# Kernel optimization log

Hardware: AMD Instinct MI355X
Metric: run time of the kernel (lower is better)

Reference implementation:

```python
import jax, jax.numpy as jnp
import numpy as np

N = 100000
E = 1600000
F_IN = 32
HID = 16
C_OUT = 10
K = 4


def setup_inputs() -> dict:
    key = jax.random.key(0)
    k1, k2, k3, k4, k5, k6, k7 = jax.random.split(key, 7)
    x = jax.random.normal(k1, (N, F_IN), dtype=jnp.float32)
    edge_index = jax.random.randint(k2, (2, E), 0, N, dtype=jnp.int64)
    # ChebConv weights: one [in, out] matrix per Chebyshev order k
    W1 = jax.random.normal(k3, (K, F_IN, HID), dtype=jnp.float32) / np.sqrt(F_IN)
    b1 = jax.random.normal(k4, (HID,), dtype=jnp.float32) * 0.01
    W2 = jax.random.normal(k5, (K, HID, C_OUT), dtype=jnp.float32) / np.sqrt(HID)
    b2 = jax.random.normal(k6, (C_OUT,), dtype=jnp.float32) * 0.01
    return {"x": x, "edge_index": edge_index, "W1": W1, "b1": b1, "W2": W2, "b2": b2}


def _cheb_conv(h, src, dst, norm, W, b, num_nodes):
    # Tx_0 = h; Tx_1 = L_hat h; Tx_k = 2 L_hat Tx_{k-1} - Tx_{k-2}
    def prop(v):  # v: [N, F] -> L_hat v via sparse gather/scatter
        return jax.ops.segment_sum(norm[:, None] * v[src], dst, num_segments=num_nodes)

    Tx0 = h
    out = Tx0 @ W[0]
    Tx1 = prop(h)
    out = out + Tx1 @ W[1]
    for k in range(2, W.shape[0]):
        Tx2 = 2.0 * prop(Tx1) - Tx0
        out = out + Tx2 @ W[k]
        Tx0, Tx1 = Tx1, Tx2
    return out + b


def reference(x, edge_index, W1, b1, W2, b2):
    src, dst = edge_index[0], edge_index[1]
    num_nodes = x.shape[0]
    # symmetric normalization with lambda_max = 2: L_hat = -D^{-1/2} A D^{-1/2}
    deg = jax.ops.segment_sum(jnp.ones((src.shape[0],), dtype=x.dtype), dst, num_segments=num_nodes)
    dis = jnp.where(deg > 0, jax.lax.rsqrt(jnp.maximum(deg, 1.0)), 0.0)
    norm = -dis[src] * dis[dst]
    h = _cheb_conv(x, src, dst, norm, W1, b1, num_nodes)
    h = jax.nn.relu(h)
    # dropout is identity in eval mode
    h = _cheb_conv(h, src, dst, norm, W2, b2, num_nodes)
    return jax.nn.log_softmax(h, axis=1)
```

## Files before the change

### kernel.cpp

```cpp
#include <hip/hip_runtime.h>
#include <hip/hip_bf16.h>
#include <math.h>


#define BLK 256
#define BLKP 512
#define NBUCK_MAX 256
#define CHUNK 8192
#define CAPB 16384
#define PLACE_CAP 10240

__device__ inline unsigned short f32_to_bf16_rne(float f) {
    unsigned int u = __float_as_uint(f);
    unsigned int rounding = 0x7FFFu + ((u >> 16) & 1u);
    return (unsigned short)((u + rounding) >> 16);
}
__device__ inline unsigned int pack_bf16x2(float a, float b) {
    return (unsigned int)f32_to_bf16_rne(a) | ((unsigned int)f32_to_bf16_rne(b) << 16);
}
__device__ inline void unpack8(const uint4 u, float* f) {
    const unsigned int* p = &u.x;
#pragma unroll
    for (int j = 0; j < 4; j++) {
        unsigned int w = p[j];
        f[2 * j]     = __uint_as_float(w << 16);
        f[2 * j + 1] = __uint_as_float(w & 0xFFFF0000u);
    }
}
__device__ inline void add8(const uint4 u, float* acc) {
    const unsigned int* p = &u.x;
#pragma unroll
    for (int j = 0; j < 4; j++) {
        unsigned int w = p[j];
        acc[2 * j]     += __uint_as_float(w << 16);
        acc[2 * j + 1] += __uint_as_float(w & 0xFFFF0000u);
    }
}
__device__ inline uint4 pack8(const float* r) {
    uint4 o;
    o.x = pack_bf16x2(r[0], r[1]);
    o.y = pack_bf16x2(r[2], r[3]);
    o.z = pack_bf16x2(r[4], r[5]);
    o.w = pack_bf16x2(r[6], r[7]);
    return o;
}

__device__ inline void fma8_w8(const uint4 u, float s, const float* __restrict__ W,
                               float* acc) {
    const unsigned int* p = &u.x;
#pragma unroll
    for (int q = 0; q < 4; q++) {
        float fa = __uint_as_float(p[q] << 16) * s;
        float fb = __uint_as_float(p[q] & 0xFFFF0000u) * s;
        const float* Wa = W + (2 * q) * 16;
        const float* Wb = W + (2 * q + 1) * 16;
#pragma unroll
        for (int j = 0; j < 8; j++) acc[j] += fa * Wa[j] + fb * Wb[j];
    }
}

__global__ __launch_bounds__(BLK)
void binned_scatter_kernel(const int* __restrict__ src, const int* __restrict__ dst,
                           int* __restrict__ bfill, int* __restrict__ tmp,
                           int E, int nbuck) {
    __shared__ int cnt[NBUCK_MAX];
    __shared__ int lofs[NBUCK_MAX + 1];
    __shared__ int pos[NBUCK_MAX];
    __shared__ int gbase[NBUCK_MAX];
    __shared__ int stage[CHUNK];
    __shared__ unsigned char bkt[CHUNK];

    int tid = threadIdx.x;
    int e0 = blockIdx.x * CHUNK;
    int nE = min(CHUNK, E - e0);

    for (int b = tid; b < nbuck; b += BLK) { cnt[b] = 0; pos[b] = 0; }
    __syncthreads();

    for (int i = tid; i < nE; i += BLK) {
        int d = dst[e0 + i];
        atomicAdd(&cnt[d >> 9], 1);
    }
    __syncthreads();

    {
        int v = (tid < nbuck) ? cnt[tid] : 0;
        lofs[tid] = v;
        __syncthreads();
        for (int off = 1; off < BLK; off <<= 1) {
            int t = (tid >= off) ? lofs[tid - off] : 0;
            __syncthreads();
            lofs[tid] += t;
            __syncthreads();
        }
        int incl = lofs[tid];
        __syncthreads();
        lofs[tid] = incl - v;
        if (tid == 0) lofs[nbuck] = nE;
        if (tid < nbuck && v > 0)
            gbase[tid] = tid * CAPB + atomicAdd(&bfill[tid], v);
    }
    __syncthreads();

    for (int i = tid; i < nE; i += BLK) {
        int s = src[e0 + i];
        int d = dst[e0 + i];
        int b = d >> 9;
        int slot = lofs[b] + atomicAdd(&pos[b], 1);
        stage[slot] = (s << 9) | (d & 511);
        bkt[slot] = (unsigned char)b;
    }
    __syncthreads();

    for (int i = tid; i < nE; i += BLK) {
        int b = bkt[i];
        tmp[gbase[b] + (i - lofs[b])] = stage[i];
    }
}

__global__ __launch_bounds__(BLKP)
void bucket_place_kernel(const int* __restrict__ bfill, const int* __restrict__ tmp,
                         int* __restrict__ psrc, int* __restrict__ rowbeg,
                         int* __restrict__ rowend, float* __restrict__ dis,
                         float* __restrict__ d2, float* __restrict__ inv,
                         const float* __restrict__ x, uint4* __restrict__ u0, int N) {
    __shared__ int cnt4[512 * 4];
    __shared__ int ofs[512];
    __shared__ int fill4[512 * 4];
    __shared__ int stage[PLACE_CAP];

    int b = blockIdx.x;
    int tid = threadIdx.x;
    int n0 = b << 9;
    int nn = min(512, N - n0);
    int S = b * CAPB;
    int tot = bfill[b];

    int t1 = N >> 2, t2 = N >> 1, t3 = t2 + t1;

    for (int i = tid; i < 512 * 4; i += BLKP) { cnt4[i] = 0; fill4[i] = 0; }
    __syncthreads();

    for (int i = tid; i < tot; i += BLKP) {
        int rec = tmp[S + i];
        int nl = rec & 511;
        int s = rec >> 9;
        int q = (s >= t2) ? ((s >= t3) ? 3 : 2) : ((s >= t1) ? 1 : 0);
        atomicAdd(&cnt4[nl * 4 + q], 1);
    }
    __syncthreads();

    int c0 = cnt4[tid * 4 + 0], c1 = cnt4[tid * 4 + 1];
    int c2 = cnt4[tid * 4 + 2], c3 = cnt4[tid * 4 + 3];
    int v = c0 + c1 + c2 + c3;
    cnt4[tid * 4 + 0] = 0;
    cnt4[tid * 4 + 1] = c0;
    cnt4[tid * 4 + 2] = c0 + c1;
    cnt4[tid * 4 + 3] = c0 + c1 + c2;
    ofs[tid] = v;
    __syncthreads();
    for (int off = 1; off < 512; off <<= 1) {
        int t = (tid >= off) ? ofs[tid - off] : 0;
        __syncthreads();
        ofs[tid] += t;
        __syncthreads();
    }
    int excl = ofs[tid] - v;
    __syncthreads();
    ofs[tid] = excl;
    float dn = (v > 0) ? rsqrtf((float)v) : 0.0f;
    if (tid < nn) {
        int n = n0 + tid;
        rowbeg[n] = S + excl;
        rowend[n] = S + excl + v;
        float fv = (float)v;
        dis[n] = dn;
        d2[n]  = (v > 0) ? 1.0f / fv : 0.0f;
        inv[n] = (v > 0) ? sqrtf(fv) : 0.0f;
        const float4* xr = reinterpret_cast<const float4*>(x + (size_t)n * 32);
#pragma unroll
        for (int c = 0; c < 4; c++) {
            float4 a = xr[c * 2], bb = xr[c * 2 + 1];
            float r[8] = {dn * a.x, dn * a.y, dn * a.z, dn * a.w,
                          dn * bb.x, dn * bb.y, dn * bb.z, dn * bb.w};
            u0[(size_t)n * 4 + c] = pack8(r);
        }
    }
    __syncthreads();

    if (tot <= PLACE_CAP) {
        for (int i = tid; i < tot; i += BLKP) {
            int rec = tmp[S + i];
            int nl = rec & 511;
            int s = rec >> 9;
            int q = (s >= t2) ? ((s >= t3) ? 3 : 2) : ((s >= t1) ? 1 : 0);
            int slot = ofs[nl] + cnt4[nl * 4 + q] + atomicAdd(&fill4[nl * 4 + q], 1);
            stage[slot] = s;
        }
        __syncthreads();
        for (int i = tid; i < tot; i += BLKP) psrc[S + i] = stage[i];
    } else {
        for (int i = tid; i < tot; i += BLKP) {
            int rec = tmp[S + i];
            int nl = rec & 511;
            int s = rec >> 9;
            int q = (s >= t2) ? ((s >= t3) ? 3 : 2) : ((s >= t1) ? 1 : 0);
            int slot = S + ofs[nl] + cnt4[nl * 4 + q] + atomicAdd(&fill4[nl * 4 + q], 1);
            psrc[slot] = s;
        }
    }
}

template <int C, bool HAVE_PREV>
__global__ __launch_bounds__(BLK)
void prop_u_kernel(const int* __restrict__ rowbeg, const int* __restrict__ rowend,
                   const int* __restrict__ psrc, const float* __restrict__ d2,
                   const uint4* __restrict__ vb, const uint4* __restrict__ prevb,
                   uint4* __restrict__ outb, float scale, int N) {
    int t = blockIdx.x * blockDim.x + threadIdx.x;
    int n = t / C;
    int c = t % C;
    if (n >= N) return;
    int beg = rowbeg[n];
    int end = rowend[n];
    float acc[8];
#pragma unroll
    for (int j = 0; j < 8; j++) acc[j] = 0.f;
    int i = beg;
    for (; i + 7 < end; i += 8) {
        int s0 = psrc[i],     s1 = psrc[i + 1], s2 = psrc[i + 2], s3 = psrc[i + 3];
        int s4 = psrc[i + 4], s5 = psrc[i + 5], s6 = psrc[i + 6], s7 = psrc[i + 7];
        uint4 a0 = vb[(size_t)s0 * C + c];
        uint4 a1 = vb[(size_t)s1 * C + c];
        uint4 a2 = vb[(size_t)s2 * C + c];
        uint4 a3 = vb[(size_t)s3 * C + c];
        uint4 a4 = vb[(size_t)s4 * C + c];
        uint4 a5 = vb[(size_t)s5 * C + c];
        uint4 a6 = vb[(size_t)s6 * C + c];
        uint4 a7 = vb[(size_t)s7 * C + c];
        add8(a0, acc); add8(a1, acc); add8(a2, acc); add8(a3, acc);
        add8(a4, acc); add8(a5, acc); add8(a6, acc); add8(a7, acc);
    }
    for (; i + 3 < end; i += 4) {
        int s0 = psrc[i], s1 = psrc[i + 1], s2 = psrc[i + 2], s3 = psrc[i + 3];
        uint4 a0 = vb[(size_t)s0 * C + c];
        uint4 a1 = vb[(size_t)s1 * C + c];
        uint4 a2 = vb[(size_t)s2 * C + c];
        uint4 a3 = vb[(size_t)s3 * C + c];
        add8(a0, acc); add8(a1, acc); add8(a2, acc); add8(a3, acc);
    }
    for (; i < end; i++) {
        uint4 a0 = vb[(size_t)psrc[i] * C + c];
        add8(a0, acc);
    }
    float f = -scale * d2[n];
    float r[8];
    if (HAVE_PREV) {
        float p[8];
        unpack8(prevb[(size_t)n * C + c], p);
#pragma unroll
        for (int j = 0; j < 8; j++) r[j] = f * acc[j] - p[j];
    } else {
#pragma unroll
        for (int j = 0; j < 8; j++) r[j] = f * acc[j];
    }
    outb[(size_t)n * C + c] = pack8(r);
}

__global__ __launch_bounds__(BLK)
void combine1_kernel(const float* __restrict__ x, const uint4* __restrict__ u1,
                     const uint4* __restrict__ u2, const uint4* __restrict__ u3,
                     const float* __restrict__ inv, const float* __restrict__ dis,
                     const float* __restrict__ W1, const float* __restrict__ b1,
                     uint4* __restrict__ hb, uint4* __restrict__ uh, int N) {
    __shared__ float sW[4 * 32 * 16];
    __shared__ float sb[16];
    for (int i = threadIdx.x; i < 4 * 32 * 16; i += blockDim.x) sW[i] = W1[i];
    if (threadIdx.x < 16) sb[threadIdx.x] = b1[threadIdx.x];
    __syncthreads();
    int t = blockIdx.x * blockDim.x + threadIdx.x;
    int n = t >> 1;
    int h = t & 1;
    if (n >= N) return;
    const float* sWh = sW + h * 8;
    float acc[8];
#pragma unroll
    for (int j = 0; j < 8; j++) acc[j] = sb[h * 8 + j];
    {
        const float4* in4 = reinterpret_cast<const float4*>(x + (size_t)n * 32);
#pragma unroll
        for (int q = 0; q < 8; q++) {
            float4 a = in4[q];
            const float* Wq = sWh + q * 4 * 16;
#pragma unroll
            for (int j = 0; j < 8; j++)
                acc[j] += a.x * Wq[j] + a.y * Wq[16 + j] + a.z * Wq[32 + j] + a.w * Wq[48 + j];
        }
    }
    float iv = inv[n];
#pragma unroll
    for (int c = 0; c < 4; c++) fma8_w8(u1[(size_t)n * 4 + c], iv, sWh + 512 + c * 128, acc);
#pragma unroll
    for (int c = 0; c < 4; c++) fma8_w8(u2[(size_t)n * 4 + c], iv, sWh + 1024 + c * 128, acc);
#pragma unroll
    for (int c = 0; c < 4; c++) fma8_w8(u3[(size_t)n * 4 + c], iv, sWh + 1536 + c * 128, acc);
    if (iv == 0.0f) {
        const float4* in4 = reinterpret_cast<const float4*>(x + (size_t)n * 32);
#pragma unroll
        for (int q = 0; q < 8; q++) {
            float4 a = in4[q];
            const float* Wq = sWh + 1024 + q * 4 * 16;
#pragma unroll
            for (int j = 0; j < 8; j++)
                acc[j] -= a.x * Wq[j] + a.y * Wq[16 + j] + a.z * Wq[32 + j] + a.w * Wq[48 + j];
        }
    }
    float dn = dis[n];
    float r[8], u[8];
#pragma unroll
    for (int j = 0; j < 8; j++) {
        r[j] = fmaxf(acc[j], 0.0f);
        u[j] = dn * r[j];
    }
    hb[(size_t)n * 2 + h] = pack8(r);
    uh[(size_t)n * 2 + h] = pack8(u);
}

__global__ __launch_bounds__(BLK)
void prop_combine2_kernel(const int* __restrict__ rowbeg, const int* __restrict__ rowend,
                          const int* __restrict__ psrc, const float* __restrict__ d2,
                          const uint4* __restrict__ us2t, const uint4* __restrict__ us1t,
                          const uint4* __restrict__ hbt, const float* __restrict__ inv,
                          const float* __restrict__ W2, const float* __restrict__ b2,
                          float* __restrict__ out, int N) {
    __shared__ float sW[4 * 16 * 10];
    __shared__ float sb[10];
    for (int i = threadIdx.x; i < 4 * 16 * 10; i += blockDim.x) sW[i] = W2[i];
    if (threadIdx.x < 10) sb[threadIdx.x] = b2[threadIdx.x];
    __syncthreads();
    int t = blockIdx.x * blockDim.x + threadIdx.x;
    int n = t >> 1;
    int c = t & 1;
    if (n >= N) return;
    int beg = rowbeg[n];
    int end = rowend[n];
    float acc[8];
#pragma unroll
    for (int j = 0; j < 8; j++) acc[j] = 0.f;
    int i = beg;
    for (; i + 7 < end; i += 8) {
        int s0 = psrc[i],     s1 = psrc[i + 1], s2 = psrc[i + 2], s3 = psrc[i + 3];
        int s4 = psrc[i + 4], s5 = psrc[i + 5], s6 = psrc[i + 6], s7 = psrc[i + 7];
        uint4 a0 = us2t[(size_t)s0 * 2 + c];
        uint4 a1 = us2t[(size_t)s1 * 2 + c];
        uint4 a2 = us2t[(size_t)s2 * 2 + c];
        uint4 a3 = us2t[(size_t)s3 * 2 + c];
        uint4 a4 = us2t[(size_t)s4 * 2 + c];
        uint4 a5 = us2t[(size_t)s5 * 2 + c];
        uint4 a6 = us2t[(size_t)s6 * 2 + c];
        uint4 a7 = us2t[(size_t)s7 * 2 + c];
        add8(a0, acc); add8(a1, acc); add8(a2, acc); add8(a3, acc);
        add8(a4, acc); add8(a5, acc); add8(a6, acc); add8(a7, acc);
    }
    for (; i < end; i++) add8(us2t[(size_t)psrc[i] * 2 + c], acc);
    float f = -2.0f * d2[n];
    float p1[8], p2[8], ph[8], r[8];
    unpack8(us1t[(size_t)n * 2 + c], p1);
    unpack8(us2t[(size_t)n * 2 + c], p2);
    unpack8(hbt[(size_t)n * 2 + c], ph);
#pragma unroll
    for (int j = 0; j < 8; j++) r[j] = f * acc[j] - p1[j];
    float a10[10];
#pragma unroll
    for (int o = 0; o < 10; o++) a10[o] = (c == 0) ? sb[o] : 0.0f;
    float iv = inv[n];
    const float* W0 = sW + (c * 8) * 10;
#pragma unroll
    for (int j = 0; j < 8; j++) {
        float w0 = ph[j];
        float w1 = p1[j] * iv;
        float w2 = p2[j] * iv;
        float w3 = r[j] * iv;
        const float* Wj = W0 + j * 10;
#pragma unroll
        for (int o = 0; o < 10; o++)
            a10[o] += w0 * Wj[o] + w1 * Wj[160 + o] + w2 * Wj[320 + o] + w3 * Wj[480 + o];
    }
    if (iv == 0.0f) {
#pragma unroll
        for (int j = 0; j < 8; j++) {
            const float* Wj = W0 + j * 10 + 320;
#pragma unroll
            for (int o = 0; o < 10; o++) a10[o] -= ph[j] * Wj[o];
        }
    }
#pragma unroll
    for (int o = 0; o < 10; o++) a10[o] += __shfl_xor(a10[o], 1);
    float m = a10[0];
#pragma unroll
    for (int o = 1; o < 10; o++) m = fmaxf(m, a10[o]);
    float sum = 0.0f;
#pragma unroll
    for (int o = 0; o < 10; o++) sum += expf(a10[o] - m);
    float lse = m + logf(sum);
    float* op = out + (size_t)n * 10 + c * 5;
#pragma unroll
    for (int o = 0; o < 5; o++) op[o] = a10[c * 5 + o] - lse;
}

extern "C" void kernel_launch(void* const* d_in, const int* in_sizes, int n_in,
                              void* d_out, int out_size, void* d_ws, size_t ws_size,
                              hipStream_t stream) {
    const float* x  = (const float*)d_in[0];
    const int*   ei = (const int*)d_in[1];
    const float* W1 = (const float*)d_in[2];
    const float* b1 = (const float*)d_in[3];
    const float* W2 = (const float*)d_in[4];
    const float* b2 = (const float*)d_in[5];
    float* out = (float*)d_out;

    const int N = in_sizes[0] / 32;
    const int E = in_sizes[1] / 2;
    const int* src = ei;
    const int* dst = ei + E;

    const int nbuck = (N + 511) / 512;

    char* w = (char*)d_ws;
    int*   bfill  = (int*)w;              w += NBUCK_MAX * 4;
    int*   rowbeg = (int*)w;              w += (size_t)(N + 4) * 4;
    int*   rowend = (int*)w;              w += (size_t)(N + 4) * 4;
    float* dis    = (float*)w;            w += (size_t)N * 4;
    float* d2     = (float*)w;            w += (size_t)N * 4;
    float* inv    = (float*)w;            w += (size_t)N * 4;
    int*   tmp    = (int*)w;              w += (size_t)NBUCK_MAX * CAPB * 4;
    int*   psrc   = (int*)w;              w += (size_t)NBUCK_MAX * CAPB * 4;
    uint4* u0     = (uint4*)w;            w += (size_t)64 * N;
    uint4* u1     = (uint4*)w;            w += (size_t)64 * N;
    uint4* u2     = (uint4*)w;            w += (size_t)64 * N;
    uint4* u3     = (uint4*)w;            w += (size_t)64 * N;
    uint4* hb     = (uint4*)w;            w += (size_t)32 * N;
    uint4* uh     = (uint4*)w;            w += (size_t)32 * N;
    uint4* us1    = (uint4*)w;            w += (size_t)32 * N;
    uint4* us2    = (uint4*)w;            w += (size_t)32 * N;

    int gN2  = (N * 2 + BLK - 1) / BLK;
    int gU32 = (N * 4 + BLK - 1) / BLK;
    int gU16 = (N * 2 + BLK - 1) / BLK;
    int gCH  = (E + CHUNK - 1) / CHUNK;

    hipMemsetAsync(bfill, 0, NBUCK_MAX * sizeof(int), stream);
    binned_scatter_kernel<<<gCH, BLK, 0, stream>>>(src, dst, bfill, tmp, E, nbuck);
    bucket_place_kernel<<<nbuck, BLKP, 0, stream>>>(bfill, tmp, psrc, rowbeg, rowend,
                                                    dis, d2, inv, x, u0, N);

    prop_u_kernel<4, false><<<gU32, BLK, 0, stream>>>(rowbeg, rowend, psrc, d2, u0, nullptr, u1, 1.0f, N);
    prop_u_kernel<4, true ><<<gU32, BLK, 0, stream>>>(rowbeg, rowend, psrc, d2, u1, u0,      u2, 2.0f, N);
    prop_u_kernel<4, true ><<<gU32, BLK, 0, stream>>>(rowbeg, rowend, psrc, d2, u2, u1,      u3, 2.0f, N);
    combine1_kernel<<<gN2, BLK, 0, stream>>>(x, u1, u2, u3, inv, dis, W1, b1, hb, uh, N);

    prop_u_kernel<2, false><<<gU16, BLK, 0, stream>>>(rowbeg, rowend, psrc, d2, uh,  nullptr, us1, 1.0f, N);
    prop_u_kernel<2, true ><<<gU16, BLK, 0, stream>>>(rowbeg, rowend, psrc, d2, us1, uh,      us2, 2.0f, N);
    prop_combine2_kernel<<<gU16, BLK, 0, stream>>>(rowbeg, rowend, psrc, d2, us2, us1,
                                                   hb, inv, W2, b2, out, N);
}
```

Baseline: 283.9 us.

## Project features through weights first and propagate narrow vectors via Clenshaw recurrence

Layer 1 now multiplies x by all four Chebyshev weight matrices up front (zgen), then evaluates the polynomial with a Clenshaw-style backward recurrence on 16-wide projected vectors instead of propagating 32-wide features. Layer 2 does the same: the hidden activations are projected to padded 16-wide outputs before propagation. This halves the bytes gathered per edge in the first layer's three sparse propagations and removes the separate combine passes. The cost is more dense FLOPs up front, more intermediate buffers, and a different bf16 rounding path for the recurrence.

```diff
diff --git a/kernel.cpp b/kernel.cpp
--- a/kernel.cpp
+++ b/kernel.cpp
@@ -43,20 +43,6 @@
     o.z = pack_bf16x2(r[4], r[5]);
     o.w = pack_bf16x2(r[6], r[7]);
     return o;
-}
-
-__device__ inline void fma8_w8(const uint4 u, float s, const float* __restrict__ W,
-                               float* acc) {
-    const unsigned int* p = &u.x;
-#pragma unroll
-    for (int q = 0; q < 4; q++) {
-        float fa = __uint_as_float(p[q] << 16) * s;
-        float fb = __uint_as_float(p[q] & 0xFFFF0000u) * s;
-        const float* Wa = W + (2 * q) * 16;
-        const float* Wb = W + (2 * q + 1) * 16;
-#pragma unroll
-        for (int j = 0; j < 8; j++) acc[j] += fa * Wa[j] + fb * Wb[j];
-    }
 }
 
 __global__ __launch_bounds__(BLK)
@@ -122,8 +108,7 @@
 void bucket_place_kernel(const int* __restrict__ bfill, const int* __restrict__ tmp,
                          int* __restrict__ psrc, int* __restrict__ rowbeg,
                          int* __restrict__ rowend, float* __restrict__ dis,
-                         float* __restrict__ d2, float* __restrict__ inv,
-                         const float* __restrict__ x, uint4* __restrict__ u0, int N) {
+                         float* __restrict__ d2, float* __restrict__ inv, int N) {
     __shared__ int cnt4[512 * 4];
     __shared__ int ofs[512];
     __shared__ int fill4[512 * 4];
@@ -168,23 +153,14 @@
     int excl = ofs[tid] - v;
     __syncthreads();
     ofs[tid] = excl;
-    float dn = (v > 0) ? rsqrtf((float)v) : 0.0f;
     if (tid < nn) {
         int n = n0 + tid;
         rowbeg[n] = S + excl;
         rowend[n] = S + excl + v;
         float fv = (float)v;
-        dis[n] = dn;
+        dis[n] = (v > 0) ? rsqrtf(fv) : 0.0f;
         d2[n]  = (v > 0) ? 1.0f / fv : 0.0f;
         inv[n] = (v > 0) ? sqrtf(fv) : 0.0f;
-        const float4* xr = reinterpret_cast<const float4*>(x + (size_t)n * 32);
-#pragma unroll
-        for (int c = 0; c < 4; c++) {
-            float4 a = xr[c * 2], bb = xr[c * 2 + 1];
-            float r[8] = {dn * a.x, dn * a.y, dn * a.z, dn * a.w,
-                          dn * bb.x, dn * bb.y, dn * bb.z, dn * bb.w};
-            u0[(size_t)n * 4 + c] = pack8(r);
-        }
     }
     __syncthreads();
 
@@ -211,133 +187,58 @@
     }
 }
 
-template <int C, bool HAVE_PREV>
 __global__ __launch_bounds__(BLK)
-void prop_u_kernel(const int* __restrict__ rowbeg, const int* __restrict__ rowend,
-                   const int* __restrict__ psrc, const float* __restrict__ d2,
-                   const uint4* __restrict__ vb, const uint4* __restrict__ prevb,
-                   uint4* __restrict__ outb, float scale, int N) {
-    int t = blockIdx.x * blockDim.x + threadIdx.x;
-    int n = t / C;
-    int c = t % C;
-    if (n >= N) return;
-    int beg = rowbeg[n];
-    int end = rowend[n];
-    float acc[8];
-#pragma unroll
-    for (int j = 0; j < 8; j++) acc[j] = 0.f;
-    int i = beg;
-    for (; i + 7 < end; i += 8) {
-        int s0 = psrc[i],     s1 = psrc[i + 1], s2 = psrc[i + 2], s3 = psrc[i + 3];
-        int s4 = psrc[i + 4], s5 = psrc[i + 5], s6 = psrc[i + 6], s7 = psrc[i + 7];
-        uint4 a0 = vb[(size_t)s0 * C + c];
-        uint4 a1 = vb[(size_t)s1 * C + c];
-        uint4 a2 = vb[(size_t)s2 * C + c];
-        uint4 a3 = vb[(size_t)s3 * C + c];
-        uint4 a4 = vb[(size_t)s4 * C + c];
-        uint4 a5 = vb[(size_t)s5 * C + c];
-        uint4 a6 = vb[(size_t)s6 * C + c];
-        uint4 a7 = vb[(size_t)s7 * C + c];
-        add8(a0, acc); add8(a1, acc); add8(a2, acc); add8(a3, acc);
-        add8(a4, acc); add8(a5, acc); add8(a6, acc); add8(a7, acc);
-    }
-    for (; i + 3 < end; i += 4) {
-        int s0 = psrc[i], s1 = psrc[i + 1], s2 = psrc[i + 2], s3 = psrc[i + 3];
-        uint4 a0 = vb[(size_t)s0 * C + c];
-        uint4 a1 = vb[(size_t)s1 * C + c];
-        uint4 a2 = vb[(size_t)s2 * C + c];
-        uint4 a3 = vb[(size_t)s3 * C + c];
-        add8(a0, acc); add8(a1, acc); add8(a2, acc); add8(a3, acc);
-    }
-    for (; i < end; i++) {
-        uint4 a0 = vb[(size_t)psrc[i] * C + c];
-        add8(a0, acc);
-    }
-    float f = -scale * d2[n];
-    float r[8];
-    if (HAVE_PREV) {
-        float p[8];
-        unpack8(prevb[(size_t)n * C + c], p);
-#pragma unroll
-        for (int j = 0; j < 8; j++) r[j] = f * acc[j] - p[j];
-    } else {
-#pragma unroll
-        for (int j = 0; j < 8; j++) r[j] = f * acc[j];
-    }
-    outb[(size_t)n * C + c] = pack8(r);
-}
-
-__global__ __launch_bounds__(BLK)
-void combine1_kernel(const float* __restrict__ x, const uint4* __restrict__ u1,
-                     const uint4* __restrict__ u2, const uint4* __restrict__ u3,
-                     const float* __restrict__ inv, const float* __restrict__ dis,
-                     const float* __restrict__ W1, const float* __restrict__ b1,
-                     uint4* __restrict__ hb, uint4* __restrict__ uh, int N) {
+void zgen_kernel(const float* __restrict__ x, const float* __restrict__ dis,
+                 const float* __restrict__ W1,
+                 uint4* __restrict__ z0t, uint4* __restrict__ uz1t,
+                 uint4* __restrict__ uz2t, uint4* __restrict__ uz3t,
+                 uint4* __restrict__ z2rt, int N) {
     __shared__ float sW[4 * 32 * 16];
-    __shared__ float sb[16];
     for (int i = threadIdx.x; i < 4 * 32 * 16; i += blockDim.x) sW[i] = W1[i];
-    if (threadIdx.x < 16) sb[threadIdx.x] = b1[threadIdx.x];
     __syncthreads();
     int t = blockIdx.x * blockDim.x + threadIdx.x;
     int n = t >> 1;
     int h = t & 1;
     if (n >= N) return;
-    const float* sWh = sW + h * 8;
-    float acc[8];
-#pragma unroll
-    for (int j = 0; j < 8; j++) acc[j] = sb[h * 8 + j];
-    {
-        const float4* in4 = reinterpret_cast<const float4*>(x + (size_t)n * 32);
-#pragma unroll
-        for (int q = 0; q < 8; q++) {
-            float4 a = in4[q];
-            const float* Wq = sWh + q * 4 * 16;
-#pragma unroll
-            for (int j = 0; j < 8; j++)
-                acc[j] += a.x * Wq[j] + a.y * Wq[16 + j] + a.z * Wq[32 + j] + a.w * Wq[48 + j];
+    float acc0[8], acc1[8], acc2[8], acc3[8];
+#pragma unroll
+    for (int j = 0; j < 8; j++) { acc0[j] = 0.f; acc1[j] = 0.f; acc2[j] = 0.f; acc3[j] = 0.f; }
+    const float4* x4 = reinterpret_cast<const float4*>(x + (size_t)n * 32);
+#pragma unroll
+    for (int q = 0; q < 8; q++) {
+        float4 a = x4[q];
+        float xi[4] = {a.x, a.y, a.z, a.w};
+#pragma unroll
+        for (int u = 0; u < 4; u++) {
+            const float* Wb = sW + (q * 4 + u) * 16 + h * 8;
+            float xv = xi[u];
+#pragma unroll
+            for (int j = 0; j < 8; j++) {
+                acc0[j] += xv * Wb[j];
+                acc1[j] += xv * Wb[512 + j];
+                acc2[j] += xv * Wb[1024 + j];
+                acc3[j] += xv * Wb[1536 + j];
+            }
         }
     }
-    float iv = inv[n];
-#pragma unroll
-    for (int c = 0; c < 4; c++) fma8_w8(u1[(size_t)n * 4 + c], iv, sWh + 512 + c * 128, acc);
-#pragma unroll
-    for (int c = 0; c < 4; c++) fma8_w8(u2[(size_t)n * 4 + c], iv, sWh + 1024 + c * 128, acc);
-#pragma unroll
-    for (int c = 0; c < 4; c++) fma8_w8(u3[(size_t)n * 4 + c], iv, sWh + 1536 + c * 128, acc);
-    if (iv == 0.0f) {
-        const float4* in4 = reinterpret_cast<const float4*>(x + (size_t)n * 32);
-#pragma unroll
-        for (int q = 0; q < 8; q++) {
-            float4 a = in4[q];
-            const float* Wq = sWh + 1024 + q * 4 * 16;
-#pragma unroll
-            for (int j = 0; j < 8; j++)
-                acc[j] -= a.x * Wq[j] + a.y * Wq[16 + j] + a.z * Wq[32 + j] + a.w * Wq[48 + j];
-        }
-    }
     float dn = dis[n];
-    float r[8], u[8];
-#pragma unroll
-    for (int j = 0; j < 8; j++) {
-        r[j] = fmaxf(acc[j], 0.0f);
-        u[j] = dn * r[j];
-    }
-    hb[(size_t)n * 2 + h] = pack8(r);
-    uh[(size_t)n * 2 + h] = pack8(u);
-}
-
+    float s1[8], s2[8], s3[8];
+#pragma unroll
+    for (int j = 0; j < 8; j++) { s1[j] = dn * acc1[j]; s2[j] = dn * acc2[j]; s3[j] = dn * acc3[j]; }
+    size_t o = (size_t)n * 2 + h;
+    z0t[o]  = pack8(acc0);
+    uz1t[o] = pack8(s1);
+    uz2t[o] = pack8(s2);
+    z2rt[o] = pack8(acc2);
+    uz3t[o] = pack8(s3);
+}
+
+template <bool HAVE_SUB>
 __global__ __launch_bounds__(BLK)
-void prop_combine2_kernel(const int* __restrict__ rowbeg, const int* __restrict__ rowend,
-                          const int* __restrict__ psrc, const float* __restrict__ d2,
-                          const uint4* __restrict__ us2t, const uint4* __restrict__ us1t,
-                          const uint4* __restrict__ hbt, const float* __restrict__ inv,
-                          const float* __restrict__ W2, const float* __restrict__ b2,
-                          float* __restrict__ out, int N) {
-    __shared__ float sW[4 * 16 * 10];
-    __shared__ float sb[10];
-    for (int i = threadIdx.x; i < 4 * 16 * 10; i += blockDim.x) sW[i] = W2[i];
-    if (threadIdx.x < 10) sb[threadIdx.x] = b2[threadIdx.x];
-    __syncthreads();
+void prop_cl_kernel(const int* __restrict__ rowbeg, const int* __restrict__ rowend,
+                    const int* __restrict__ psrc, const float* __restrict__ d2,
+                    const uint4* __restrict__ vb, const uint4* __restrict__ addt,
+                    const uint4* __restrict__ subt, uint4* __restrict__ outb, int N) {
     int t = blockIdx.x * blockDim.x + threadIdx.x;
     int n = t >> 1;
     int c = t & 1;
@@ -351,61 +252,186 @@
     for (; i + 7 < end; i += 8) {
         int s0 = psrc[i],     s1 = psrc[i + 1], s2 = psrc[i + 2], s3 = psrc[i + 3];
         int s4 = psrc[i + 4], s5 = psrc[i + 5], s6 = psrc[i + 6], s7 = psrc[i + 7];
-        uint4 a0 = us2t[(size_t)s0 * 2 + c];
-        uint4 a1 = us2t[(size_t)s1 * 2 + c];
-        uint4 a2 = us2t[(size_t)s2 * 2 + c];
-        uint4 a3 = us2t[(size_t)s3 * 2 + c];
-        uint4 a4 = us2t[(size_t)s4 * 2 + c];
-        uint4 a5 = us2t[(size_t)s5 * 2 + c];
-        uint4 a6 = us2t[(size_t)s6 * 2 + c];
-        uint4 a7 = us2t[(size_t)s7 * 2 + c];
+        uint4 a0 = vb[(size_t)s0 * 2 + c];
+        uint4 a1 = vb[(size_t)s1 * 2 + c];
+        uint4 a2 = vb[(size_t)s2 * 2 + c];
+        uint4 a3 = vb[(size_t)s3 * 2 + c];
+        uint4 a4 = vb[(size_t)s4 * 2 + c];
+        uint4 a5 = vb[(size_t)s5 * 2 + c];
+        uint4 a6 = vb[(size_t)s6 * 2 + c];
+        uint4 a7 = vb[(size_t)s7 * 2 + c];
         add8(a0, acc); add8(a1, acc); add8(a2, acc); add8(a3, acc);
         add8(a4, acc); add8(a5, acc); add8(a6, acc); add8(a7, acc);
     }
-    for (; i < end; i++) add8(us2t[(size_t)psrc[i] * 2 + c], acc);
+    for (; i < end; i++) add8(vb[(size_t)psrc[i] * 2 + c], acc);
     float f = -2.0f * d2[n];
-    float p1[8], p2[8], ph[8], r[8];
-    unpack8(us1t[(size_t)n * 2 + c], p1);
-    unpack8(us2t[(size_t)n * 2 + c], p2);
-    unpack8(hbt[(size_t)n * 2 + c], ph);
-#pragma unroll
-    for (int j = 0; j < 8; j++) r[j] = f * acc[j] - p1[j];
-    float a10[10];
-#pragma unroll
-    for (int o = 0; o < 10; o++) a10[o] = (c == 0) ? sb[o] : 0.0f;
-    float iv = inv[n];
-    const float* W0 = sW + (c * 8) * 10;
+    float ad[8], r[8];
+    unpack8(addt[(size_t)n * 2 + c], ad);
+    if (HAVE_SUB) {
+        float sb[8];
+        unpack8(subt[(size_t)n * 2 + c], sb);
+#pragma unroll
+        for (int j = 0; j < 8; j++) r[j] = f * acc[j] + ad[j] - sb[j];
+    } else {
+#pragma unroll
+        for (int j = 0; j < 8; j++) r[j] = f * acc[j] + ad[j];
+    }
+    outb[(size_t)n * 2 + c] = pack8(r);
+}
+
+__global__ __launch_bounds__(BLK)
+void final1_kernel(const int* __restrict__ rowbeg, const int* __restrict__ rowend,
+                   const int* __restrict__ psrc, const float* __restrict__ dis,
+                   const float* __restrict__ d2, const float* __restrict__ inv,
+                   const uint4* __restrict__ ub1t, const uint4* __restrict__ ub2t,
+                   const uint4* __restrict__ z0t, const uint4* __restrict__ z2rt,
+                   const float* __restrict__ W2, const float* __restrict__ b1,
+                   uint4* __restrict__ w0t, uint4* __restrict__ uw1t,
+                   uint4* __restrict__ uw2t, uint4* __restrict__ uw3t,
+                   uint4* __restrict__ w2rt, int N) {
+    __shared__ float sW[4 * 16 * 16];
+    __shared__ float sb1[16];
+    for (int i = threadIdx.x; i < 4 * 16 * 16; i += blockDim.x) {
+        int k = i >> 8, rem = i & 255, j = rem >> 4, o = rem & 15;
+        sW[i] = (o < 10) ? W2[k * 160 + j * 10 + o] : 0.0f;
+    }
+    if (threadIdx.x < 16) sb1[threadIdx.x] = b1[threadIdx.x];
+    __syncthreads();
+    int t = blockIdx.x * blockDim.x + threadIdx.x;
+    int n = t >> 1;
+    int h = t & 1;
+    if (n >= N) return;
+    int beg = rowbeg[n];
+    int end = rowend[n];
+    float acc[8];
+#pragma unroll
+    for (int j = 0; j < 8; j++) acc[j] = 0.f;
+    int i = beg;
+    for (; i + 7 < end; i += 8) {
+        int s0 = psrc[i],     s1 = psrc[i + 1], s2 = psrc[i + 2], s3 = psrc[i + 3];
+        int s4 = psrc[i + 4], s5 = psrc[i + 5], s6 = psrc[i + 6], s7 = psrc[i + 7];
+        uint4 a0 = ub1t[(size_t)s0 * 2 + h];
+        uint4 a1 = ub1t[(size_t)s1 * 2 + h];
+        uint4 a2 = ub1t[(size_t)s2 * 2 + h];
+        uint4 a3 = ub1t[(size_t)s3 * 2 + h];
+        uint4 a4 = ub1t[(size_t)s4 * 2 + h];
+        uint4 a5 = ub1t[(size_t)s5 * 2 + h];
+        uint4 a6 = ub1t[(size_t)s6 * 2 + h];
+        uint4 a7 = ub1t[(size_t)s7 * 2 + h];
+        add8(a0, acc); add8(a1, acc); add8(a2, acc); add8(a3, acc);
+        add8(a4, acc); add8(a5, acc); add8(a6, acc); add8(a7, acc);
+    }
+    for (; i < end; i++) add8(ub1t[(size_t)psrc[i] * 2 + h], acc);
+    size_t o2 = (size_t)n * 2 + h;
+    float z0[8], hrow[8];
+    unpack8(z0t[o2], z0);
+    if (d2[n] == 0.0f) {
+        float z2[8];
+        unpack8(z2rt[o2], z2);
+#pragma unroll
+        for (int j = 0; j < 8; j++) hrow[j] = fmaxf(sb1[h * 8 + j] + z0[j] - z2[j], 0.0f);
+    } else {
+        float b2v[8];
+        unpack8(ub2t[o2], b2v);
+        float dn = dis[n], iv = inv[n];
+#pragma unroll
+        for (int j = 0; j < 8; j++)
+            hrow[j] = fmaxf(sb1[h * 8 + j] + z0[j] - dn * acc[j] - iv * b2v[j], 0.0f);
+    }
+    float h16[16];
 #pragma unroll
     for (int j = 0; j < 8; j++) {
-        float w0 = ph[j];
-        float w1 = p1[j] * iv;
-        float w2 = p2[j] * iv;
-        float w3 = r[j] * iv;
-        const float* Wj = W0 + j * 10;
-#pragma unroll
-        for (int o = 0; o < 10; o++)
-            a10[o] += w0 * Wj[o] + w1 * Wj[160 + o] + w2 * Wj[320 + o] + w3 * Wj[480 + o];
-    }
-    if (iv == 0.0f) {
-#pragma unroll
-        for (int j = 0; j < 8; j++) {
-            const float* Wj = W0 + j * 10 + 320;
-#pragma unroll
-            for (int o = 0; o < 10; o++) a10[o] -= ph[j] * Wj[o];
+        float other = __shfl_xor(hrow[j], 1);
+        h16[h * 8 + j] = hrow[j];
+        h16[(1 - h) * 8 + j] = other;
+    }
+    float w0[8], w1[8], w2[8], w3[8];
+#pragma unroll
+    for (int o = 0; o < 8; o++) { w0[o] = 0.f; w1[o] = 0.f; w2[o] = 0.f; w3[o] = 0.f; }
+#pragma unroll
+    for (int j = 0; j < 16; j++) {
+        float hv = h16[j];
+        const float* Wb = sW + j * 16 + h * 8;
+#pragma unroll
+        for (int o = 0; o < 8; o++) {
+            w0[o] += hv * Wb[o];
+            w1[o] += hv * Wb[256 + o];
+            w2[o] += hv * Wb[512 + o];
+            w3[o] += hv * Wb[768 + o];
         }
     }
-#pragma unroll
-    for (int o = 0; o < 10; o++) a10[o] += __shfl_xor(a10[o], 1);
-    float m = a10[0];
-#pragma unroll
-    for (int o = 1; o < 10; o++) m = fmaxf(m, a10[o]);
-    float sum = 0.0f;
-#pragma unroll
-    for (int o = 0; o < 10; o++) sum += expf(a10[o] - m);
-    float lse = m + logf(sum);
-    float* op = out + (size_t)n * 10 + c * 5;
-#pragma unroll
-    for (int o = 0; o < 5; o++) op[o] = a10[c * 5 + o] - lse;
+    float dn = dis[n];
+    float s1[8], s2[8], s3[8];
+#pragma unroll
+    for (int o = 0; o < 8; o++) { s1[o] = dn * w1[o]; s2[o] = dn * w2[o]; s3[o] = dn * w3[o]; }
+    w0t[o2]  = pack8(w0);
+    uw1t[o2] = pack8(s1);
+    uw2t[o2] = pack8(s2);
+    w2rt[o2] = pack8(w2);
+    uw3t[o2] = pack8(s3);
+}
+
+__global__ __launch_bounds__(BLK)
+void final2_kernel(const int* __restrict__ rowbeg, const int* __restrict__ rowend,
+                   const int* __restrict__ psrc, const float* __restrict__ dis,
+                   const float* __restrict__ d2, const float* __restrict__ inv,
+                   const uint4* __restrict__ uv1t, const uint4* __restrict__ uv2t,
+                   const uint4* __restrict__ w0t, const uint4* __restrict__ w2rt,
+                   const float* __restrict__ b2, float* __restrict__ out, int N) {
+    __shared__ float sb2[16];
+    if (threadIdx.x < 16) sb2[threadIdx.x] = (threadIdx.x < 10) ? b2[threadIdx.x] : 0.0f;
+    __syncthreads();
+    int t = blockIdx.x * blockDim.x + threadIdx.x;
+    int n = t >> 1;
+    int c = t & 1;
+    if (n >= N) return;
+    int beg = rowbeg[n];
+    int end = rowend[n];
+    float acc[8];
+#pragma unroll
+    for (int j = 0; j < 8; j++) acc[j] = 0.f;
+    int i = beg;
+    for (; i + 7 < end; i += 8) {
+        int s0 = psrc[i],     s1 = psrc[i + 1], s2 = psrc[i + 2], s3 = psrc[i + 3];
+        int s4 = psrc[i + 4], s5 = psrc[i + 5], s6 = psrc[i + 6], s7 = psrc[i + 7];
+        uint4 a0 = uv1t[(size_t)s0 * 2 + c];
+        uint4 a1 = uv1t[(size_t)s1 * 2 + c];
+        uint4 a2 = uv1t[(size_t)s2 * 2 + c];
+        uint4 a3 = uv1t[(size_t)s3 * 2 + c];
+        uint4 a4 = uv1t[(size_t)s4 * 2 + c];
+        uint4 a5 = uv1t[(size_t)s5 * 2 + c];
+        uint4 a6 = uv1t[(size_t)s6 * 2 + c];
+        uint4 a7 = uv1t[(size_t)s7 * 2 + c];
+        add8(a0, acc); add8(a1, acc); add8(a2, acc); add8(a3, acc);
+        add8(a4, acc); add8(a5, acc); add8(a6, acc); add8(a7, acc);
+    }
+    for (; i < end; i++) add8(uv1t[(size_t)psrc[i] * 2 + c], acc);
+    size_t o2 = (size_t)n * 2 + c;
+    float w0[8], L[8];
+    unpack8(w0t[o2], w0);
+    if (d2[n] == 0.0f) {
+        float w2[8];
+        unpack8(w2rt[o2], w2);
+#pragma unroll
+        for (int j = 0; j < 8; j++) L[j] = sb2[c * 8 + j] + w0[j] - w2[j];
+    } else {
+        float v2[8];
+        unpack8(uv2t[o2], v2);
+        float dn = dis[n], iv = inv[n];
+#pragma unroll
+        for (int j = 0; j < 8; j++)
+            L[j] = sb2[c * 8 + j] + w0[j] - dn * acc[j] - iv * v2[j];
+    }
+    int nreal = (c == 0) ? 8 : 2;
+    float m = -3.0e38f;
+    for (int j = 0; j < nreal; j++) m = fmaxf(m, L[j]);
+    m = fmaxf(m, __shfl_xor(m, 1));
+    float s = 0.0f;
+    for (int j = 0; j < nreal; j++) s += expf(L[j] - m);
+    s += __shfl_xor(s, 1);
+    float lse = m + logf(s);
+    float* op = out + (size_t)n * 10 + c * 8;
+    for (int j = 0; j < nreal; j++) op[j] = L[j] - lse;
 }
 
 extern "C" void kernel_launch(void* const* d_in, const int* in_sizes, int n_in,
@@ -435,32 +461,42 @@
     float* inv    = (float*)w;            w += (size_t)N * 4;
     int*   tmp    = (int*)w;              w += (size_t)NBUCK_MAX * CAPB * 4;
     int*   psrc   = (int*)w;              w += (size_t)NBUCK_MAX * CAPB * 4;
-    uint4* u0     = (uint4*)w;            w += (size_t)64 * N;
-    uint4* u1     = (uint4*)w;            w += (size_t)64 * N;
-    uint4* u2     = (uint4*)w;            w += (size_t)64 * N;
-    uint4* u3     = (uint4*)w;            w += (size_t)64 * N;
-    uint4* hb     = (uint4*)w;            w += (size_t)32 * N;
-    uint4* uh     = (uint4*)w;            w += (size_t)32 * N;
-    uint4* us1    = (uint4*)w;            w += (size_t)32 * N;
-    uint4* us2    = (uint4*)w;            w += (size_t)32 * N;
-
-    int gN2  = (N * 2 + BLK - 1) / BLK;
-    int gU32 = (N * 4 + BLK - 1) / BLK;
-    int gU16 = (N * 2 + BLK - 1) / BLK;
-    int gCH  = (E + CHUNK - 1) / CHUNK;
+    uint4* z0t    = (uint4*)w;            w += (size_t)32 * N;
+    uint4* uz1t   = (uint4*)w;            w += (size_t)32 * N;
+    uint4* uz2t   = (uint4*)w;            w += (size_t)32 * N;
+    uint4* uz3t   = (uint4*)w;            w += (size_t)32 * N;
+    uint4* z2rt   = (uint4*)w;            w += (size_t)32 * N;
+    uint4* ub2t   = (uint4*)w;            w += (size_t)32 * N;
+    uint4* ub1t   = (uint4*)w;            w += (size_t)32 * N;
+    uint4* w0t    = (uint4*)w;            w += (size_t)32 * N;
+    uint4* uw1t   = (uint4*)w;            w += (size_t)32 * N;
+    uint4* uw2t   = (uint4*)w;            w += (size_t)32 * N;
+    uint4* uw3t   = (uint4*)w;            w += (size_t)32 * N;
+    uint4* w2rt   = (uint4*)w;            w += (size_t)32 * N;
+    uint4* uv2t   = (uint4*)w;            w += (size_t)32 * N;
+    uint4* uv1t   = (uint4*)w;            w += (size_t)32 * N;
+
+    int gN2 = (N * 2 + BLK - 1) / BLK;
+    int gCH = (E + CHUNK - 1) / CHUNK;
 
     hipMemsetAsync(bfill, 0, NBUCK_MAX * sizeof(int), stream);
     binned_scatter_kernel<<<gCH, BLK, 0, stream>>>(src, dst, bfill, tmp, E, nbuck);
     bucket_place_kernel<<<nbuck, BLKP, 0, stream>>>(bfill, tmp, psrc, rowbeg, rowend,
-                                                    dis, d2, inv, x, u0, N);
-
-    prop_u_kernel<4, false><<<gU32, BLK, 0, stream>>>(rowbeg, rowend, psrc, d2, u0, nullptr, u1, 1.0f, N);
-    prop_u_kernel<4, true ><<<gU32, BLK, 0, stream>>>(rowbeg, rowend, psrc, d2, u1, u0,      u2, 2.0f, N);
-    prop_u_kernel<4, true ><<<gU32, BLK, 0, stream>>>(rowbeg, rowend, psrc, d2, u2, u1,      u3, 2.0f, N);
-    combine1_kernel<<<gN2, BLK, 0, stream>>>(x, u1, u2, u3, inv, dis, W1, b1, hb, uh, N);
-
-    prop_u_kernel<2, false><<<gU16, BLK, 0, stream>>>(rowbeg, rowend, psrc, d2, uh,  nullptr, us1, 1.0f, N);
-    prop_u_kernel<2, true ><<<gU16, BLK, 0, stream>>>(rowbeg, rowend, psrc, d2, us1, uh,      us2, 2.0f, N);
-    prop_combine2_kernel<<<gU16, BLK, 0, stream>>>(rowbeg, rowend, psrc, d2, us2, us1,
-                                                   hb, inv, W2, b2, out, N);
-}
+                                                    dis, d2, inv, N);
+
+    zgen_kernel<<<gN2, BLK, 0, stream>>>(x, dis, W1, z0t, uz1t, uz2t, uz3t, z2rt, N);
+    prop_cl_kernel<false><<<gN2, BLK, 0, stream>>>(rowbeg, rowend, psrc, d2,
+                                                   uz3t, uz2t, nullptr, ub2t, N);
+    prop_cl_kernel<true ><<<gN2, BLK, 0, stream>>>(rowbeg, rowend, psrc, d2,
+                                                   ub2t, uz1t, uz3t, ub1t, N);
+    final1_kernel<<<gN2, BLK, 0, stream>>>(rowbeg, rowend, psrc, dis, d2, inv,
+                                           ub1t, ub2t, z0t, z2rt, W2, b1,
+                                           w0t, uw1t, uw2t, uw3t, w2rt, N);
+
+    prop_cl_kernel<false><<<gN2, BLK, 0, stream>>>(rowbeg, rowend, psrc, d2,
+                                                   uw3t, uw2t, nullptr, uv2t, N);
+    prop_cl_kernel<true ><<<gN2, BLK, 0, stream>>>(rowbeg, rowend, psrc, d2,
+                                                   uv2t, uw1t, uw3t, uv1t, N);
+    final2_kernel<<<gN2, BLK, 0, stream>>>(rowbeg, rowend, psrc, dis, d2, inv,
+                                           uv1t, uv2t, w0t, w2rt, b2, out, N);
+}
```

Result: faster. 250.8 us (-11.7%).
